# Kernel optimization log

Hardware: AMD Instinct MI355X
Metric: run time of the kernel (lower is better)

Reference implementation:

```python
import jax, jax.numpy as jnp
import numpy as np

W = 5; WW = 25; STEP = 8; DF = 128; NH = 8; DH = 16; EPS = 1e-5


def sinusoid_pe(ww, d):
    pos = np.arange(ww)[:, None].astype(np.float32)
    div = np.exp(np.arange(0, d, 2).astype(np.float32) * (-np.log(10000.0) / d))
    pe = np.zeros((ww, d), np.float32)
    pe[:, 0::2] = np.sin(pos * div)
    pe[:, 1::2] = np.cos(pos * div)
    return jnp.asarray(pe)


def ln(x, s, b):
    m = x.mean(-1, keepdims=True)
    v = ((x - m) ** 2).mean(-1, keepdims=True)
    return (x - m) / jnp.sqrt(v + EPS) * s + b


def attn_layer(x, src, wq, wk, wv, wm, m1w, m1b, m2w, m2b, n1s, n1b, n2s, n2b):
    N, T, D = x.shape
    q = (x @ wq).reshape(N, T, NH, DH)
    k = (src @ wk).reshape(N, T, NH, DH)
    v = (src @ wv).reshape(N, T, NH, DH)
    a = jax.nn.softmax(jnp.einsum('nqhd,nkhd->nhqk', q, k) * (DH ** -0.5), axis=-1)
    msg = jnp.einsum('nhqk,nkhd->nqhd', a, v).reshape(N, T, D) @ wm
    msg = ln(msg, n1s, n1b)
    h = jnp.concatenate([x, msg], axis=-1)
    h = jax.nn.relu(h @ m1w + m1b) @ m2w + m2b
    return x + ln(h, n2s, n2b)


def local_transformer(x0, x1, P):
    names = ['self', 'cross', 'self', 'cross']
    for i, nm in enumerate(names):
        p = tuple(a[i] for a in P)
        if nm == 'self':
            x0 = attn_layer(x0, x0, *p)
            x1 = attn_layer(x1, x1, *p)
        else:
            x0 = attn_layer(x0, x1, *p)
            x1 = attn_layer(x1, x0, *p)
    return x0, x1


def unfold_window(fm):
    # F.unfold(kernel=5, stride=4, pad=2) then 'B (C MM) L -> B L MM C'
    B, C, H, Wd = fm.shape
    pat = jax.lax.conv_general_dilated_patches(fm, (W, W), (4, 4), [(W // 2, W // 2)] * 2)
    Ho, Wo = pat.shape[2], pat.shape[3]
    pat = pat.reshape(B, C, WW, Ho * Wo)  # channel-major ordering matches torch unfold
    return pat.transpose(0, 3, 2, 1)  # [B, L, WW, C]


def forward(mdesc0, mdesc1, fine0, fine1, conv_w, conv_b, proj_w, proj_b,
            merge_w, merge_b, reg1_w, reg1_b, reg2_w, reg2_b, reg_w, reg_b,
            lt_wq, lt_wk, lt_wv, lt_wm, lt_m1w, lt_m1b, lt_m2w, lt_m2b,
            lt_n1s, lt_n1b, lt_n2s, lt_n2b):
    B, L, Dc = mdesc0.shape
    Wc = int(np.sqrt(L))
    # dual-softmax confidence matrix
    sim = jnp.einsum('bld,bmd->blm', mdesc0 / Dc, mdesc1 / Dc) / 0.1
    cm = jax.nn.softmax(sim, axis=1) * jax.nn.softmax(sim, axis=2)
    # mutual nearest-neighbor filter (static-shape: keep all B*L rows + mask)
    mut = (cm == cm.max(axis=2, keepdims=True)) & (cm == cm.max(axis=1, keepdims=True))
    cf = cm * mut
    mask = cf.max(axis=2) > 0  # [B, L]
    j = jnp.argmax(cf, axis=2)  # [B, L]
    # 1x1 conv to fine dim
    f0 = jnp.einsum('bchw,oc->bohw', fine0, conv_w[:, :, 0, 0]) + conv_b[None, :, None, None]
    f1 = jnp.einsum('bchw,oc->bohw', fine1, conv_w[:, :, 0, 0]) + conv_b[None, :, None, None]
    u0 = unfold_window(f0)
    u1 = unfold_window(f1)  # [B, L, WW, DF]
    N = B * L
    b_all = jnp.repeat(jnp.arange(B), L)
    idx1 = b_all * L + j.reshape(-1)
    local0 = u0.reshape(N, WW, DF)
    local1 = u1.reshape(N, WW, DF)[idx1]
    c0 = mdesc0.reshape(N, Dc)
    c1 = mdesc1.reshape(N, Dc)[idx1]
    local = jnp.concatenate([local0, local1], axis=0)  # [2N, WW, DF]
    center = jnp.concatenate([c0, c1], axis=0) @ proj_w + proj_b  # [2N, DF]
    center = jnp.broadcast_to(center[:, None, :], (2 * N, WW, DF))
    ld = jnp.concatenate([local, center], axis=-1) @ merge_w + merge_b
    ld = ld + sinusoid_pe(WW, DF)[None]
    d0, d1 = ld[:N], ld[N:]
    P = (lt_wq, lt_wk, lt_wv, lt_wm, lt_m1w, lt_m1b, lt_m2w, lt_m2b, lt_n1s, lt_n1b, lt_n2s, lt_n2b)
    fd0, fd1 = local_transformer(d0, d1, P)
    c = WW // 2
    cen = jnp.broadcast_to(fd0[:, c:c + 1, :], (N, WW, DF))
    feat = jnp.concatenate([cen, fd1], axis=-1)  # [N, WW, 2*DF]
    feat = feat @ reg1_w + reg1_b  # [N, WW, DF]
    feat = feat.reshape(N, WW * DF)  # [N, 3200]
    feat = feat @ reg2_w + reg2_b  # dropout is identity at eval
    coords = feat @ reg_w + reg_b  # [N, 2]
    xj = (j % Wc) * STEP
    yj = (j // Wc) * STEP
    base = jnp.stack([xj, yj], axis=-1).reshape(N, 2).astype(coords.dtype)
    return (base + coords) * mask.reshape(N, 1).astype(coords.dtype)


def setup_inputs():
    key = jax.random.key(0)
    ks = jax.random.split(key, 24)
    B, L, Dc = 2, 2304, 256
    Hf = 192
    nl = 4

    def rn(k, shape, fan):
        return jax.random.normal(k, shape, jnp.float32) * (fan ** -0.5)

    return {
        'mdesc0': jax.random.normal(ks[0], (B, L, Dc), jnp.float32),
        'mdesc1': jax.random.normal(ks[1], (B, L, Dc), jnp.float32),
        'fine0': jax.random.normal(ks[2], (B, Dc, Hf, Hf), jnp.float32),
        'fine1': jax.random.normal(ks[3], (B, Dc, Hf, Hf), jnp.float32),
        'conv_w': rn(ks[4], (DF, Dc, 1, 1), Dc),
        'conv_b': jnp.zeros((DF,), jnp.float32),
        'proj_w': rn(ks[5], (Dc, DF), Dc),
        'proj_b': jnp.zeros((DF,), jnp.float32),
        'merge_w': rn(ks[6], (2 * DF, DF), 2 * DF),
        'merge_b': jnp.zeros((DF,), jnp.float32),
        'reg1_w': rn(ks[7], (2 * DF, DF), 2 * DF),
        'reg1_b': jnp.zeros((DF,), jnp.float32),
        'reg2_w': rn(ks[8], (WW * DF, DF), WW * DF),
        'reg2_b': jnp.zeros((DF,), jnp.float32),
        'reg_w': rn(ks[9], (DF, 2), DF),
        'reg_b': jnp.zeros((2,), jnp.float32),
        'lt_wq': rn(ks[10], (nl, DF, DF), DF),
        'lt_wk': rn(ks[11], (nl, DF, DF), DF),
        'lt_wv': rn(ks[12], (nl, DF, DF), DF),
        'lt_wm': rn(ks[13], (nl, DF, DF), DF),
        'lt_m1w': rn(ks[14], (nl, 2 * DF, 2 * DF), 2 * DF),
        'lt_m1b': jnp.zeros((nl, 2 * DF), jnp.float32),
        'lt_m2w': rn(ks[15], (nl, 2 * DF, DF), 2 * DF),
        'lt_m2b': jnp.zeros((nl, DF), jnp.float32),
        'lt_n1s': jnp.ones((nl, DF), jnp.float32),
        'lt_n1b': jnp.zeros((nl, DF), jnp.float32),
        'lt_n2s': jnp.ones((nl, DF), jnp.float32),
        'lt_n2b': jnp.zeros((nl, DF), jnp.float32),
    }


def reference(mdesc0, mdesc1, fine0, fine1, conv_w, conv_b, proj_w, proj_b,
              merge_w, merge_b, reg1_w, reg1_b, reg2_w, reg2_b, reg_w, reg_b,
              lt_wq, lt_wk, lt_wv, lt_wm, lt_m1w, lt_m1b, lt_m2w, lt_m2b,
              lt_n1s, lt_n1b, lt_n2s, lt_n2b):
    return forward(mdesc0, mdesc1, fine0, fine1, conv_w, conv_b, proj_w, proj_b,
                   merge_w, merge_b, reg1_w, reg1_b, reg2_w, reg2_b, reg_w, reg_b,
                   lt_wq, lt_wk, lt_wv, lt_wm, lt_m1w, lt_m1b, lt_m2w, lt_m2b,
                   lt_n1s, lt_n1b, lt_n2s, lt_n2b)
```

## Files before the change

### kernel.cpp

```cpp
#include <hip/hip_runtime.h>
#include <stdint.h>
#include <type_traits>

#define DEVFN static __device__ __forceinline__

typedef __attribute__((ext_vector_type(8))) short bf16x8v;
typedef __attribute__((ext_vector_type(4))) float f32x4v;
typedef __attribute__((ext_vector_type(2))) _Float16 h2;

DEVFN float b2f(short s) {
  union { unsigned u; float f; } c; c.u = ((unsigned)(unsigned short)s) << 16; return c.f;
}
DEVFN short f2b(float f) {
  union { float f; unsigned u; } c; c.f = f;
  unsigned r = c.u + 0x7fffu + ((c.u >> 16) & 1u);
  return (short)(r >> 16);
}
DEVFN short f2h(float f) {
  union { _Float16 h; short s; } c; c.h = (_Float16)f; return c.s;
}
DEVFN void gl_lds16(const void* g, void* l) {
  __builtin_amdgcn_global_load_lds((const __attribute__((address_space(1))) void*)g,
                                   (__attribute__((address_space(3))) void*)l, 16, 0, 0);
}
DEVFN double exp_small(double x) {
  return 1.0 + x * (1.0 + x * (0.5 + x * ((1.0 / 6.0) + x * (1.0 / 24.0))));
}


__global__ void prep_all(const float* __restrict__ conv_w, const float* __restrict__ proj_w,
                         const float* __restrict__ merge_w, const float* __restrict__ reg1_w,
                         const float* __restrict__ reg2_w, const float* __restrict__ wq,
                         const float* __restrict__ wk, const float* __restrict__ wv,
                         const float* __restrict__ wm, const float* __restrict__ m1w,
                         const float* __restrict__ m2w,
                         short* __restrict__ convT, short* __restrict__ projT,
                         short* __restrict__ mergeAT, short* __restrict__ mergeBT,
                         short* __restrict__ reg1T, short* __restrict__ reg2T,
                         short* __restrict__ wqkvT, short* __restrict__ wmT,
                         short* __restrict__ m1T, short* __restrict__ m2T,
                         float* __restrict__ pe, short* __restrict__ zp) {
  const int L0 = 32768, L1 = 32768, L2 = 16384, L3 = 16384, L4 = 32768, L5 = 409600;
  const int L6 = 196608, L7 = 65536, L8 = 262144, L9 = 131072, L10 = 3200, L11 = 128;
  const int TOT = L0+L1+L2+L3+L4+L5+L6+L7+L8+L9+L10+L11;
  for (int gi = blockIdx.x * blockDim.x + threadIdx.x; gi < TOT; gi += gridDim.x * blockDim.x) {
    int i = gi;
    if (i < L0) { convT[i] = f2b(conv_w[i]); continue; } i -= L0;
    if (i < L1) { int n = i >> 8, k = i & 255; projT[i] = f2b(proj_w[k * 128 + n]); continue; } i -= L1;
    if (i < L2) { int n = i >> 7, k = i & 127; mergeAT[i] = f2b(merge_w[k * 128 + n]); continue; } i -= L2;
    if (i < L3) { int n = i >> 7, k = i & 127; mergeBT[i] = f2b(merge_w[(128 + k) * 128 + n]); continue; } i -= L3;
    if (i < L4) { int n = i >> 8, k = i & 255; reg1T[i] = f2b(reg1_w[k * 128 + n]); continue; } i -= L4;
    if (i < L5) { int n = i / 3200, k = i - n * 3200; reg2T[i] = f2b(reg2_w[k * 128 + n]); continue; } i -= L5;
    if (i < L6) {
      int l = i / 49152; int r = i - l * 49152; int w = r / 16384; int r2 = r - w * 16384;
      int n = r2 >> 7, k = r2 & 127;
      const float* s = (w == 0) ? wq : (w == 1) ? wk : wv;
      wqkvT[i] = f2b(s[l * 16384 + k * 128 + n]); continue;
    } i -= L6;
    if (i < L7) { int l = i >> 14; int r = i & 16383; int n = r >> 7, k = r & 127;
      wmT[i] = f2b(wm[l * 16384 + k * 128 + n]); continue; } i -= L7;
    if (i < L8) { int l = i >> 16; int r = i & 65535; int n = r >> 8, k = r & 255;
      m1T[i] = f2b(m1w[l * 65536 + k * 256 + n]); continue; } i -= L8;
    if (i < L9) { int l = i >> 15; int r = i & 32767; int n = r >> 8, k = r & 255;
      m2T[i] = f2b(m2w[l * 32768 + k * 128 + n]); continue; } i -= L9;
    if (i < L10) {
      int t = i >> 7, d = i & 127; int i2 = d >> 1;
      float div = expf(((float)(2 * i2)) * (-logf(10000.f) / 128.f));
      float ang = (float)t * div;
      pe[i] = (d & 1) ? cosf(ang) : sinf(ang); continue;
    } i -= L10;
    zp[i] = 0;
  }
}


__global__ __launch_bounds__(256) void sim_gemm(const float* __restrict__ A,
                                                const float* __restrict__ Bm,
                                                float* __restrict__ S) {
  int b = blockIdx.z;
  A += (size_t)b * 2304 * 256; Bm += (size_t)b * 2304 * 256; S += (size_t)b * 2304 * 2304;
  __shared__ float As[96][33], Bs[96][33];
  int tid = threadIdx.x;
  int tx = tid & 15, ty = tid >> 4;
  int rb = blockIdx.x * 96, cb = blockIdx.y * 96;
  float acc[6][6] = {};
  for (int k0 = 0; k0 < 256; k0 += 32) {
    #pragma unroll
    for (int s = 0; s < 3; ++s) {
      int slot = s * 256 + tid;
      int r = slot >> 3, cq = slot & 7;
      float4 va = *(const float4*)&A[(size_t)(rb + r) * 256 + k0 + 4 * cq];
      float4 vb = *(const float4*)&Bm[(size_t)(cb + r) * 256 + k0 + 4 * cq];
      As[r][4 * cq] = va.x; As[r][4 * cq + 1] = va.y; As[r][4 * cq + 2] = va.z; As[r][4 * cq + 3] = va.w;
      Bs[r][4 * cq] = vb.x; Bs[r][4 * cq + 1] = vb.y; Bs[r][4 * cq + 2] = vb.z; Bs[r][4 * cq + 3] = vb.w;
    }
    __syncthreads();
    #pragma unroll 4
    for (int k = 0; k < 32; ++k) {
      float av[6], bv[6];
      #pragma unroll
      for (int i = 0; i < 6; ++i) av[i] = As[ty + 16 * i][k];
      #pragma unroll
      for (int j = 0; j < 6; ++j) bv[j] = Bs[tx + 16 * j][k];
      #pragma unroll
      for (int i = 0; i < 6; ++i)
        #pragma unroll
        for (int j = 0; j < 6; ++j) acc[i][j] += av[i] * bv[j];
    }
    __syncthreads();
  }
  #pragma unroll
  for (int i = 0; i < 6; ++i)
    #pragma unroll
    for (int j = 0; j < 6; ++j) {
      float t = acc[i][j] * (1.0f / 65536.0f);
      S[(size_t)(rb + ty + 16 * i) * 2304 + cb + tx + 16 * j] = t / 0.1f;
    }
}

__global__ __launch_bounds__(256) void row_lse(const float* __restrict__ S, double* __restrict__ lnR) {
  int row = blockIdx.x;
  const float* Sp = S + (size_t)row * 2304;
  double a = 0;
  for (int m = threadIdx.x; m < 2304; m += 256) a += exp_small((double)Sp[m]);
  __shared__ double red[256];
  red[threadIdx.x] = a; __syncthreads();
  for (int s = 128; s > 0; s >>= 1) { if (threadIdx.x < (unsigned)s) red[threadIdx.x] += red[threadIdx.x + s]; __syncthreads(); }
  if (!threadIdx.x) lnR[row] = log(red[0]);
}

__global__ __launch_bounds__(256) void col_part(const float* __restrict__ S,
                                                const double* __restrict__ lnR,
                                                double* __restrict__ psum,
                                                double* __restrict__ pkey,
                                                int* __restrict__ pidx) {
  int bb = blockIdx.z;
  int c0 = blockIdx.x * 64;
  int rc = blockIdx.y;
  int col = c0 + (threadIdx.x & 63);
  int g = threadIdx.x >> 6;
  const float* Sp = S + (size_t)bb * 2304 * 2304;
  const double* lr = lnR + bb * 2304;
  double a = 0, best = -1e300; int bi = 1 << 30;
  int l0 = rc * 192;
  for (int t = g; t < 192; t += 4) {
    int l = l0 + t;
    double sv = (double)Sp[(size_t)l * 2304 + col];
    a += exp_small(sv);
    double k = 2.0 * sv - lr[l];
    if (k > best || (k == best && l < bi)) { best = k; bi = l; }
  }
  __shared__ double s_sum[256]; __shared__ double s_key[256]; __shared__ int s_idx[256];
  s_sum[threadIdx.x] = a; s_key[threadIdx.x] = best; s_idx[threadIdx.x] = bi;
  __syncthreads();
  if (g == 0) {
    double ts = a; double tk = best; int ti = bi;
    #pragma unroll
    for (int gg = 1; gg < 4; ++gg) {
      int o = threadIdx.x + gg * 64;
      ts += s_sum[o];
      if (s_key[o] > tk || (s_key[o] == tk && s_idx[o] < ti)) { tk = s_key[o]; ti = s_idx[o]; }
    }
    size_t off = ((size_t)bb * 12 + rc) * 2304 + col;
    psum[off] = ts; pkey[off] = tk; pidx[off] = ti;
  }
}

__global__ void col_reduce(const double* __restrict__ psum, const double* __restrict__ pkey,
                           const int* __restrict__ pidx, double* __restrict__ lnC,
                           int* __restrict__ CB) {
  int i = blockIdx.x * blockDim.x + threadIdx.x;
  if (i >= 4608) return;
  int bb = i / 2304, col = i - bb * 2304;
  double s = 0; double bk = -1e300; int bi = 1 << 30;
  for (int rc = 0; rc < 12; ++rc) {
    size_t off = ((size_t)bb * 12 + rc) * 2304 + col;
    s += psum[off];
    double k = pkey[off]; int ix = pidx[off];
    if (k > bk || (k == bk && ix < bi)) { bk = k; bi = ix; }
  }
  lnC[i] = log(s);
  CB[i] = bi;
}

__global__ __launch_bounds__(256) void row_argmax(const float* __restrict__ S,
                                                  const double* __restrict__ lnC,
                                                  int* __restrict__ J) {
  int row = blockIdx.x; int bb = row / 2304;
  const float* Sp = S + (size_t)row * 2304;
  const double* lc = lnC + bb * 2304;
  double best = -1e300; int bi = 1 << 30;
  for (int m = threadIdx.x; m < 2304; m += 256) {
    double k = 2.0 * (double)Sp[m] - lc[m];
    if (k > best || (k == best && m < bi)) { best = k; bi = m; }
  }
  __shared__ double bvs[256]; __shared__ int bis[256];
  bvs[threadIdx.x] = best; bis[threadIdx.x] = bi; __syncthreads();
  for (int s = 128; s > 0; s >>= 1) {
    if (threadIdx.x < (unsigned)s) {
      double ov = bvs[threadIdx.x + s]; int oi = bis[threadIdx.x + s];
      if (ov > bvs[threadIdx.x] || (ov == bvs[threadIdx.x] && oi < bis[threadIdx.x])) { bvs[threadIdx.x] = ov; bis[threadIdx.x] = oi; }
    }
    __syncthreads();
  }
  if (!threadIdx.x) J[row] = bis[0];
}


__global__ __launch_bounds__(256) void transpose_fine(const float* __restrict__ src, short* __restrict__ dst) {
  __shared__ float t[64][65];
  int bb = blockIdx.z, p0 = blockIdx.x * 64, c0 = blockIdx.y * 64;
  for (int i = threadIdx.x; i < 4096; i += 256) {
    int cl = i >> 6, pl = i & 63;
    t[cl][pl] = src[((size_t)(bb * 256 + c0 + cl)) * 36864 + p0 + pl];
  }
  __syncthreads();
  for (int i = threadIdx.x; i < 1024; i += 256) {
    int pl = i >> 4, cg = (i & 15) * 4;
    unsigned w0 = (unsigned short)f2b(t[cg][pl]) | ((unsigned)(unsigned short)f2b(t[cg + 1][pl]) << 16);
    unsigned w1 = (unsigned short)f2b(t[cg + 2][pl]) | ((unsigned)(unsigned short)f2b(t[cg + 3][pl]) << 16);
    int2 v; v.x = (int)w0; v.y = (int)w1;
    *(int2*)&dst[((size_t)(bb * 36864 + p0 + pl)) * 256 + c0 + cg] = v;
  }
}

__global__ void cgather(const float* __restrict__ md0, const float* __restrict__ md1,
                        const int* __restrict__ J, short* __restrict__ cbuf) {
  int total = 9216 * 256;
  for (int i = blockIdx.x * blockDim.x + threadIdx.x; i < total; i += gridDim.x * blockDim.x) {
    int w = i >> 8, c = i & 255;
    const float* src;
    if (w < 4608) src = md0 + (size_t)w * 256;
    else {
      int n = w - 4608; int bb = n / 2304;
      src = md1 + (size_t)(bb * 2304 + J[n]) * 256;
    }
    cbuf[i] = f2b(src[c]);
  }
}

__global__ void build_tab(const int* __restrict__ J, const short* __restrict__ f0c,
                          const short* __restrict__ f1c, const short* __restrict__ zp,
                          unsigned long long* __restrict__ tab) {
  int total = 230400;
  for (int i = blockIdx.x * blockDim.x + threadIdx.x; i < total; i += gridDim.x * blockDim.x) {
    int w = i / 25, t = i - w * 25;
    int bb, cell; const short* fc;
    if (w < 4608) { bb = w / 2304; cell = w - bb * 2304; fc = f0c; }
    else { int n = w - 4608; bb = n / 2304; cell = J[n]; fc = f1c; }
    int cy = cell / 48, cx = cell - cy * 48;
    int y = cy * 4 - 2 + t / 5, x = cx * 4 - 2 + t % 5;
    const short* p = (y >= 0 && y < 192 && x >= 0 && x < 192)
                   ? fc + (size_t)((bb * 192 + y) * 192 + x) * 128 : zp;
    tab[i] = (unsigned long long)(uintptr_t)p;
  }
}


constexpr int AM_LIN = 0, AM_DUAL = 1, AM_TAB = 2, AM_CEN = 3, AM_QKV = 4;
constexpr int EP_BIAS = 0, EP_BF32 = 1, EP_RELU = 2, EP_LN = 3, EP_LNRES = 4, EP_MERGE = 5, EP_PART = 6, EP_F16 = 7;

template<int AMODE, int EPI>
__global__ __launch_bounds__(256)
void gemm_bf16(const short* __restrict__ A1, const short* __restrict__ A2,
               const unsigned long long* __restrict__ tab,
               const short* __restrict__ Wt, int M, int Kd, int kstr, int K1,
               const float* __restrict__ bias, int bstride,
               const float* __restrict__ lns, const float* __restrict__ lnb,
               const short* __restrict__ resid,
               const float* __restrict__ ccp, const float* __restrict__ pep,
               short* __restrict__ outb, float* __restrict__ outf, int ldc,
               long wstride, long ostride) {
  __shared__ __align__(16) short As[128 * 64];
  __shared__ __align__(16) short Bs[128 * 64];
  __shared__ float rsum[2][128], rsq[2][128];
  int tid = threadIdx.x, lane = tid & 63, wid = tid >> 6;
  int wr = wid >> 1, wc = wid & 1;
  int nwg = gridDim.x;
  int orig = blockIdx.x;
  int qd = nwg >> 3, rm = nwg & 7;
  int xcd = orig & 7, offx = orig >> 3;
  int bx = (xcd < rm ? xcd * (qd + 1) : rm * (qd + 1) + (xcd - rm) * qd) + offx;
  int rb = bx * 128;
  int by = blockIdx.y;
  int koff = blockIdx.z * Kd;
  const short* Wsel = Wt + (size_t)by * wstride;
  const float* bsel = bias ? bias + (size_t)by * bstride : nullptr;
  short* osel_b = outb ? outb + (size_t)by * ostride : nullptr;
  float* osel_f = outf ? outf + (size_t)by * ostride : nullptr;

  f32x4v acc[4][4];
  #pragma unroll
  for (int i = 0; i < 4; ++i)
    #pragma unroll
    for (int j = 0; j < 4; ++j) acc[i][j] = (f32x4v){0.f, 0.f, 0.f, 0.f};

  for (int k0 = 0; k0 < Kd; k0 += 64) {
    #pragma unroll
    for (int q = 0; q < 4; ++q) {
      int i = (wid * 4 + q) * 64 + lane;
      int r = i >> 3, pch = i & 7;
      int c = pch ^ (r & 7);
      const short* src;
      if (AMODE == AM_LIN) {
        src = A1 + (size_t)(rb + r) * kstr + koff + k0 + c * 8;
      } else if (AMODE == AM_QKV) {
        const short* Ab = (by == 0) ? A1 : A2;
        src = Ab + (size_t)(rb + r) * kstr + k0 + c * 8;
      } else if (AMODE == AM_DUAL) {
        if (k0 < K1) src = A1 + (size_t)(rb + r) * K1 + k0 + c * 8;
        else         src = A2 + (size_t)(rb + r) * (Kd - K1) + (k0 - K1) + c * 8;
      } else if (AMODE == AM_CEN) {
        int rg = rb + r;
        if (k0 < K1) src = A1 + (size_t)((rg / 25) * 25 + 12) * K1 + k0 + c * 8;
        else         src = A2 + (size_t)rg * (Kd - K1) + (k0 - K1) + c * 8;
      } else {
        src = (const short*)(uintptr_t)tab[rb + r] + k0 + c * 8;
      }
      gl_lds16(src, &As[(size_t)i * 8]);
    }
    #pragma unroll
    for (int q = 0; q < 4; ++q) {
      int i = (wid * 4 + q) * 64 + lane;
      int r = i >> 3, pch = i & 7;
      int c = pch ^ (r & 7);
      gl_lds16(Wsel + (size_t)r * kstr + koff + k0 + c * 8, &Bs[(size_t)i * 8]);
    }
    __syncthreads();
    #pragma unroll
    for (int kk = 0; kk < 2; ++kk) {
      bf16x8v af[4], bfr[4];
      #pragma unroll
      for (int mi = 0; mi < 4; ++mi) {
        int r = wr * 64 + mi * 16 + (lane & 15);
        int c = kk * 4 + (lane >> 4);
        int pch = c ^ (r & 7);
        af[mi] = *(const bf16x8v*)&As[r * 64 + pch * 8];
      }
      #pragma unroll
      for (int ni = 0; ni < 4; ++ni) {
        int r = wc * 64 + ni * 16 + (lane & 15);
        int c = kk * 4 + (lane >> 4);
        int pch = c ^ (r & 7);
        bfr[ni] = *(const bf16x8v*)&Bs[r * 64 + pch * 8];
      }
      #pragma unroll
      for (int mi = 0; mi < 4; ++mi)
        #pragma unroll
        for (int ni = 0; ni < 4; ++ni)
          acc[mi][ni] = __builtin_amdgcn_mfma_f32_16x16x32_bf16(af[mi], bfr[ni], acc[mi][ni], 0, 0, 0);
    }
    __syncthreads();
  }

  int colloc[4];
  #pragma unroll
  for (int ni = 0; ni < 4; ++ni) colloc[ni] = wc * 64 + ni * 16 + (lane & 15);
  float bv[4];
  #pragma unroll
  for (int ni = 0; ni < 4; ++ni)
    bv[ni] = (EPI == EP_MERGE || EPI == EP_PART) ? 0.f : (bsel ? bsel[colloc[ni]] : 0.f);

  #pragma unroll
  for (int mi = 0; mi < 4; ++mi)
    #pragma unroll
    for (int ni = 0; ni < 4; ++ni)
      #pragma unroll
      for (int q = 0; q < 4; ++q) {
        float v = acc[mi][ni][q] + bv[ni];
        if (EPI == EP_RELU) v = fmaxf(v, 0.f);
        acc[mi][ni][q] = v;
      }

  if (EPI == EP_LN || EPI == EP_LNRES) {
    #pragma unroll
    for (int mi = 0; mi < 4; ++mi)
      #pragma unroll
      for (int q = 0; q < 4; ++q) {
        float s = 0.f, ss = 0.f;
        #pragma unroll
        for (int ni = 0; ni < 4; ++ni) { float v = acc[mi][ni][q]; s += v; ss += v * v; }
        s += __shfl_xor(s, 1, 64); ss += __shfl_xor(ss, 1, 64);
        s += __shfl_xor(s, 2, 64); ss += __shfl_xor(ss, 2, 64);
        s += __shfl_xor(s, 4, 64); ss += __shfl_xor(ss, 4, 64);
        s += __shfl_xor(s, 8, 64); ss += __shfl_xor(ss, 8, 64);
        int rl = wr * 64 + mi * 16 + (lane >> 4) * 4 + q;
        if ((lane & 15) == 0) { rsum[wc][rl] = s; rsq[wc][rl] = ss; }
      }
    __syncthreads();
  }

  #pragma unroll
  for (int mi = 0; mi < 4; ++mi)
    #pragma unroll
    for (int q = 0; q < 4; ++q) {
      int rl = wr * 64 + mi * 16 + (lane >> 4) * 4 + q;
      long rg = rb + rl;
      float mean = 0.f, rstd = 0.f;
      if (EPI == EP_LN || EPI == EP_LNRES) {
        float s = rsum[0][rl] + rsum[1][rl];
        float ss = rsq[0][rl] + rsq[1][rl];
        mean = s * (1.f / 128.f);
        float var = ss * (1.f / 128.f) - mean * mean;
        rstd = 1.f / sqrtf(var + 1e-5f);
      }
      int wv_ = 0, tv_ = 0;
      if (EPI == EP_MERGE) { wv_ = (int)(rg / 25); tv_ = (int)(rg - (long)wv_ * 25); }
      #pragma unroll
      for (int ni = 0; ni < 4; ++ni) {
        int cg = colloc[ni];
        float v = acc[mi][ni][q];
        if (EPI == EP_MERGE) v += ccp[(size_t)wv_ * 128 + cg] + pep[tv_ * 128 + cg];
        if (EPI == EP_LN || EPI == EP_LNRES) {
          v = (v - mean) * rstd * lns[cg] + lnb[cg];
          if (EPI == EP_LNRES) v += b2f(resid[(size_t)rg * 128 + cg]);
        }
        if (EPI == EP_BF32) osel_f[(size_t)rg * ldc + cg] = v;
        else if (EPI == EP_PART) osel_f[((size_t)blockIdx.z * M + rg) * ldc + cg] = v;
        else if (EPI == EP_F16) osel_b[(size_t)rg * ldc + cg] = f2h(v);
        else osel_b[(size_t)rg * ldc + cg] = f2b(v);
      }
    }
}

__global__ void reduce_part(const float* __restrict__ part, const float* __restrict__ bias,
                            short* __restrict__ out) {
  int i = blockIdx.x * blockDim.x + threadIdx.x;
  if (i >= 4608 * 128) return;
  int c = i & 127;
  float s = bias[c];
  #pragma unroll
  for (int z = 0; z < 5; ++z) s += part[(size_t)z * 4608 * 128 + i];
  out[i] = f2b(s);
}


__global__ __launch_bounds__(256) void attn_win(const short* __restrict__ Q,
                                                const short* __restrict__ K,
                                                const short* __restrict__ V,
                                                short* __restrict__ Mo) {
  int w = blockIdx.x;
  const short* Qg = Q + (size_t)w * 3200;
  const short* Kg = K + (size_t)w * 3200;
  const short* Vg = V + (size_t)w * 3200;
  __shared__ short Qs[25 * 136 + 8], Ks[25 * 136 + 8], Vs[25 * 136 + 8];
  int tid = threadIdx.x;
  for (int s = tid; s < 400; s += 256) {
    int r = s >> 4, ch = s & 15;
    *(int4*)&Qs[r * 136 + ch * 8] = ((const int4*)Qg)[s];
    *(int4*)&Ks[r * 136 + ch * 8] = ((const int4*)Kg)[s];
    *(int4*)&Vs[r * 136 + ch * 8] = ((const int4*)Vg)[s];
  }
  __syncthreads();

  int wid = tid >> 6, lane = tid & 63;
  int half = lane >> 5, li = lane & 31;
  int h = wid * 2 + half;
  if (li < 25) {
    int i = li;
    h2 qr[8];
    #pragma unroll
    for (int t = 0; t < 8; ++t) qr[t] = *(const h2*)&Qs[i * 136 + h * 16 + t * 2];
    float p[25];
    float mx = -1e30f;
    #pragma unroll
    for (int jx = 0; jx < 25; ++jx) {
      const short* kr = &Ks[jx * 136 + h * 16];
      float s = 0.f;
      #pragma unroll
      for (int t = 0; t < 8; ++t)
        s = __builtin_amdgcn_fdot2(qr[t], *(const h2*)&kr[t * 2], s, false);
      s *= 0.25f;
      p[jx] = s;
      mx = fmaxf(mx, s);
    }
    float sum = 0.f;
    #pragma unroll
    for (int jx = 0; jx < 25; ++jx) { float e = expf(p[jx] - mx); p[jx] = e; sum += e; }
    float inv = 1.f / sum;
    h2 o2[8];
    #pragma unroll
    for (int t = 0; t < 8; ++t) { o2[t][0] = (_Float16)0.f; o2[t][1] = (_Float16)0.f; }
    #pragma unroll
    for (int jx = 0; jx < 25; ++jx) {
      _Float16 ph = (_Float16)(p[jx] * inv);
      h2 pv; pv[0] = ph; pv[1] = ph;
      const short* vr = &Vs[jx * 136 + h * 16];
      #pragma unroll
      for (int t = 0; t < 8; ++t) o2[t] += pv * (*(const h2*)&vr[t * 2]);
    }
    int* outp = (int*)(Mo + (size_t)w * 3200 + i * 128 + h * 16);
    #pragma unroll
    for (int t = 0; t < 8; ++t) {
      unsigned lo = (unsigned short)f2b((float)o2[t][0]);
      unsigned hi = (unsigned short)f2b((float)o2[t][1]);
      outp[t] = (int)(lo | (hi << 16));
    }
  }
}


__global__ void final_reg(const short* __restrict__ fv, const float* __restrict__ regw,
                          const float* __restrict__ regb, const int* __restrict__ J,
                          const int* __restrict__ CB, float* __restrict__ out) {
  int n = blockIdx.x * blockDim.x + threadIdx.x;
  if (n >= 4608) return;
  const short* f = fv + (size_t)n * 128;
  float c0 = regb[0], c1 = regb[1];
  for (int d = 0; d < 128; ++d) { float v = b2f(f[d]); c0 += v * regw[d * 2]; c1 += v * regw[d * 2 + 1]; }
  int jv = J[n]; int bb = n / 2304;
  int msk = (CB[bb * 2304 + jv] == (n - bb * 2304)) ? 1 : 0;
  float bx = (float)((jv % 48) * 8), by = (float)((jv / 48) * 8);
  out[n * 2] = msk ? (bx + c0) : 0.f;
  out[n * 2 + 1] = msk ? (by + c1) : 0.f;
}


extern "C" void kernel_launch(void* const* d_in, const int* in_sizes, int n_in,
                              void* d_out, int out_size, void* d_ws, size_t ws_size,
                              hipStream_t stream) {
  const float* md0 = (const float*)d_in[0];
  const float* md1 = (const float*)d_in[1];
  const float* fine0 = (const float*)d_in[2];
  const float* fine1 = (const float*)d_in[3];
  const float* conv_w = (const float*)d_in[4];
  const float* conv_b = (const float*)d_in[5];
  const float* proj_w = (const float*)d_in[6];
  const float* proj_b = (const float*)d_in[7];
  const float* merge_w = (const float*)d_in[8];
  const float* merge_b = (const float*)d_in[9];
  const float* reg1_w = (const float*)d_in[10];
  const float* reg1_b = (const float*)d_in[11];
  const float* reg2_w = (const float*)d_in[12];
  const float* reg2_b = (const float*)d_in[13];
  const float* reg_w = (const float*)d_in[14];
  const float* reg_b = (const float*)d_in[15];
  const float* wq_f = (const float*)d_in[16];
  const float* wk_f = (const float*)d_in[17];
  const float* wv_f = (const float*)d_in[18];
  const float* wm_f = (const float*)d_in[19];
  const float* m1w = (const float*)d_in[20];
  const float* m1b = (const float*)d_in[21];
  const float* m2w = (const float*)d_in[22];
  const float* m2b = (const float*)d_in[23];
  const float* n1s = (const float*)d_in[24];
  const float* n1b = (const float*)d_in[25];
  const float* n2s = (const float*)d_in[26];
  const float* n2b = (const float*)d_in[27];

  char* ws = (char*)d_ws;
  const size_t SZX = (size_t)230400 * 128 * 2;
  const size_t TAILSZ = 20 * 1024 * 1024;
  int CHM = 57600;
  if (SZX + 4ull * 230400 * 256 + TAILSZ <= ws_size)      CHM = 230400;
  else if (SZX + 4ull * 115200 * 256 + TAILSZ <= ws_size) CHM = 115200;
  const size_t CHR = (size_t)CHM * 256;

  short* X  = (short*)(ws);
  char*  Rb = ws + SZX;
  short* R0 = (short*)(Rb);
  short* R1 = (short*)(Rb + CHR);
  short* R2 = (short*)(Rb + 2 * CHR);
  short* R3 = (short*)(Rb + 3 * CHR);
  float* S    = (float*)Rb;
  short* F0C  = (short*)Rb;
  short* F1C  = (short*)(Rb + (size_t)73728 * 128 * 2);
  short* FT   = X;
  short* FB   = (short*)Rb;
  float* PART = (float*)(Rb + 2 * CHR);

  char* p = ws + SZX + 4 * CHR;
  double* lnR = (double*)p; p += 4608 * 8;
  double* lnC = (double*)p; p += 4608 * 8;
  int* J = (int*)p; p += 4608 * 4;
  int* CBst = (int*)p; p += 4608 * 4;
  double* PSUM = (double*)p; p += (size_t)2 * 12 * 2304 * 8;
  double* PKEY = (double*)p; p += (size_t)2 * 12 * 2304 * 8;
  int* PIDX = (int*)p; p += (size_t)2 * 12 * 2304 * 4;
  short* CBUF = (short*)p; p += (size_t)9216 * 256 * 2;
  short* CEN = (short*)p; p += (size_t)9216 * 128 * 2;
  float* CC = (float*)p; p += (size_t)9216 * 128 * 4;
  unsigned long long* TAB = (unsigned long long*)p; p += (size_t)230400 * 8;
  float* PE = (float*)p; p += 3200 * 4;
  short* ZP = (short*)p; p += 256;
  short* convT = (short*)p; p += 128 * 256 * 2;
  short* projT = (short*)p; p += 128 * 256 * 2;
  short* mergeAT = (short*)p; p += 128 * 128 * 2;
  short* mergeBT = (short*)p; p += 128 * 128 * 2;
  short* reg1T = (short*)p; p += 128 * 256 * 2;
  short* reg2T = (short*)p; p += (size_t)128 * 3200 * 2;
  short* wqkvT = (short*)p; p += (size_t)4 * 3 * 128 * 128 * 2;
  short* wmT = (short*)p; p += 4 * 128 * 128 * 2;
  short* m1T = (short*)p; p += 4 * 256 * 256 * 2;
  short* m2T = (short*)p; p += (size_t)4 * 128 * 256 * 2;
  short* FV = (short*)p; p += (size_t)4608 * 128 * 2;

  const int TQ = 115200;

  prep_all<<<512, 256, 0, stream>>>(conv_w, proj_w, merge_w, reg1_w, reg2_w,
                                    wq_f, wk_f, wv_f, wm_f, m1w, m2w,
                                    convT, projT, mergeAT, mergeBT, reg1T, reg2T,
                                    wqkvT, wmT, m1T, m2T, PE, ZP);

  sim_gemm<<<dim3(24, 24, 2), 256, 0, stream>>>(md0, md1, S);
  row_lse<<<4608, 256, 0, stream>>>(S, lnR);
  col_part<<<dim3(36, 12, 2), 256, 0, stream>>>(S, lnR, PSUM, PKEY, PIDX);
  col_reduce<<<18, 256, 0, stream>>>(PSUM, PKEY, PIDX, lnC, CBst);
  row_argmax<<<4608, 256, 0, stream>>>(S, lnC, J);

  auto gemm = [&](auto amode, auto epi, const short* A1, const short* A2,
                  const unsigned long long* tab, const short* Wt, int M, int Kd, int kstr, int K1,
                  const float* bias, int bstride, const float* lns, const float* lnb,
                  const short* resid, const float* cc, const float* pe,
                  short* outb, float* outf, int ldc, int NB, int NZ, long wstride, long ostride) {
    constexpr int AM = decltype(amode)::value, EP = decltype(epi)::value;
    gemm_bf16<AM, EP><<<dim3(M / 128, NB, NZ), 256, 0, stream>>>(
        A1, A2, tab, Wt, M, Kd, kstr, K1, bias, bstride, lns, lnb, resid, cc, pe,
        outb, outf, ldc, wstride, ostride);
  };
  using I0 = std::integral_constant<int, 0>; using I1 = std::integral_constant<int, 1>;
  using I2 = std::integral_constant<int, 2>; using I3 = std::integral_constant<int, 3>;
  using I4 = std::integral_constant<int, 4>;
  using E0 = std::integral_constant<int, 0>; using E1 = std::integral_constant<int, 1>;
  using E2 = std::integral_constant<int, 2>; using E3 = std::integral_constant<int, 3>;
  using E4 = std::integral_constant<int, 4>; using E5 = std::integral_constant<int, 5>;
  using E6 = std::integral_constant<int, 6>; using E7 = std::integral_constant<int, 7>;

  transpose_fine<<<dim3(576, 4, 2), 256, 0, stream>>>(fine0, FT);
  gemm(I0{}, E0{}, FT, nullptr, nullptr, convT, 73728, 256, 256, 0, conv_b, 0, nullptr, nullptr, nullptr, nullptr, nullptr, F0C, nullptr, 128, 1, 1, 0, 0);
  transpose_fine<<<dim3(576, 4, 2), 256, 0, stream>>>(fine1, FT);
  gemm(I0{}, E0{}, FT, nullptr, nullptr, convT, 73728, 256, 256, 0, conv_b, 0, nullptr, nullptr, nullptr, nullptr, nullptr, F1C, nullptr, 128, 1, 1, 0, 0);

  cgather<<<4608, 256, 0, stream>>>(md0, md1, J, CBUF);
  gemm(I0{}, E0{}, CBUF, nullptr, nullptr, projT, 9216, 256, 256, 0, proj_b, 0, nullptr, nullptr, nullptr, nullptr, nullptr, CEN, nullptr, 128, 1, 1, 0, 0);
  gemm(I0{}, E1{}, CEN, nullptr, nullptr, mergeBT, 9216, 128, 128, 0, merge_b, 0, nullptr, nullptr, nullptr, nullptr, nullptr, nullptr, CC, 128, 1, 1, 0, 0);
  build_tab<<<900, 256, 0, stream>>>(J, F0C, F1C, ZP, TAB);
  gemm(I2{}, E5{}, nullptr, nullptr, TAB, mergeAT, 230400, 128, 128, 0, nullptr, 0, nullptr, nullptr, nullptr, CC, PE, X, nullptr, 128, 1, 1, 0, 0);

  auto pass = [&](int i, const short* xq, const short* xkv, short* xout, int Mtotal) {
    const short* wqkv = wqkvT + (size_t)i * 3 * 16384;
    const short* wm = wmT + i * 16384;
    const short* m1 = m1T + i * 65536;
    const short* m2 = m2T + i * 32768;
    for (int off = 0; off < Mtotal; off += CHM) {
      int Mc = (Mtotal - off < CHM) ? (Mtotal - off) : CHM;
      const short* xqc = xq + (size_t)off * 128;
      const short* xkvc = xkv + (size_t)off * 128;
      gemm(I4{}, E7{}, xqc, xkvc, nullptr, wqkv, Mc, 128, 128, 0, nullptr, 0, nullptr, nullptr, nullptr, nullptr, nullptr, R0, nullptr, 128, 3, 1, 16384, (long)CHM * 128);
      attn_win<<<Mc / 25, 256, 0, stream>>>(R0, R1, R2, R0);
      gemm(I0{}, E3{}, R0, nullptr, nullptr, wm, Mc, 128, 128, 0, nullptr, 0, n1s + i * 128, n1b + i * 128, nullptr, nullptr, nullptr, R3, nullptr, 128, 1, 1, 0, 0);
      gemm(I1{}, E2{}, xqc, R3, nullptr, m1, Mc, 256, 256, 128, m1b + i * 256, 128, nullptr, nullptr, nullptr, nullptr, nullptr, R0, nullptr, 256, 2, 1, 128 * 256, 128);
      gemm(I0{}, E4{}, R0, nullptr, nullptr, m2, Mc, 256, 256, 0, m2b + i * 128, 0, n2s + i * 128, n2b + i * 128, xqc, nullptr, nullptr, xout + (size_t)off * 128, nullptr, 128, 1, 1, 0, 0);
    }
  };
  short* X1 = X + (size_t)TQ * 128;
  for (int i = 0; i < 4; ++i) {
    if ((i & 1) == 0) {
      pass(i, X, X, X, 230400);
    } else {
      pass(i, X, X1, X, TQ);
      pass(i, X1, X, X1, TQ);
    }
  }

  gemm(I3{}, E0{}, X, X1, nullptr, reg1T, TQ, 256, 256, 128, reg1_b, 0, nullptr, nullptr, nullptr, nullptr, nullptr, FB, nullptr, 128, 1, 1, 0, 0);
  gemm(I0{}, E6{}, FB, nullptr, nullptr, reg2T, 4608, 640, 3200, 0, nullptr, 0, nullptr, nullptr, nullptr, nullptr, nullptr, nullptr, PART, 128, 1, 5, 0, 0);
  reduce_part<<<2304, 256, 0, stream>>>(PART, reg2_b, FV);
  final_reg<<<18, 256, 0, stream>>>(FV, reg_w, reg_b, J, CBst, (float*)d_out);
}
```

Before: 1.772 ms.

## Fuse MLP up/down projections with LayerNorm residual into one kernel

Replaces the two GEMM launches for the attention-layer MLP (concat[x,msg]·m1 + relu, then ·m2 + bias, LayerNorm and residual) with one kernel. Each 64-row block keeps the 256-wide hidden activation in LDS in two 128-column halves and accumulates the second GEMM directly, so the hidden tensor never goes through global memory. In exchange the GEMM tiling is hand-written with less pipelining, and Mc must be a multiple of 64 since the grid is Mc/64 with no tail handling. In-place output (xout == xqc) is safe only if each block reads its own x rows before writing them.

Result: faster. 1.669 ms (-5.8%).

```diff
diff --git a/kernel.cpp b/kernel.cpp
--- a/kernel.cpp
+++ b/kernel.cpp
@@ -435,6 +435,184 @@
 }
 
 
+__global__ __launch_bounds__(256)
+void mlp_fused(const short* __restrict__ x, const short* __restrict__ msg,
+               const short* __restrict__ m1wT, const short* __restrict__ m2wT,
+               const float* __restrict__ b1, const float* __restrict__ b2,
+               const float* __restrict__ lns, const float* __restrict__ lnb,
+               short* __restrict__ out) {
+  __shared__ __align__(16) short As[64 * 64];
+  __shared__ __align__(16) short Bs[128 * 64];
+  __shared__ __align__(16) short Hs[64 * 128];
+  __shared__ float rsum[2][64], rsq[2][64];
+  int tid = threadIdx.x, lane = tid & 63, wid = tid >> 6;
+  int wr = wid >> 1, wc = wid & 1;
+  int nwg = gridDim.x;
+  int orig = blockIdx.x;
+  int qd = nwg >> 3, rm = nwg & 7;
+  int xcd = orig & 7, offx = orig >> 3;
+  int bx = (xcd < rm ? xcd * (qd + 1) : rm * (qd + 1) + (xcd - rm) * qd) + offx;
+  int rb = bx * 64;
+
+  f32x4v acc2[2][4];
+  #pragma unroll
+  for (int i = 0; i < 2; ++i)
+    #pragma unroll
+    for (int j = 0; j < 4; ++j) acc2[i][j] = (f32x4v){0.f, 0.f, 0.f, 0.f};
+
+  #pragma unroll
+  for (int nh = 0; nh < 2; ++nh) {
+    f32x4v acc1[2][4];
+    #pragma unroll
+    for (int i = 0; i < 2; ++i)
+      #pragma unroll
+      for (int j = 0; j < 4; ++j) acc1[i][j] = (f32x4v){0.f, 0.f, 0.f, 0.f};
+
+    for (int k0 = 0; k0 < 256; k0 += 64) {
+      #pragma unroll
+      for (int q = 0; q < 2; ++q) {
+        int i = (wid * 2 + q) * 64 + lane;
+        int r = i >> 3, pch = i & 7;
+        int c = pch ^ (r & 7);
+        const short* src = (k0 < 128)
+            ? x + (size_t)(rb + r) * 128 + k0 + c * 8
+            : msg + (size_t)(rb + r) * 128 + (k0 - 128) + c * 8;
+        gl_lds16(src, &As[(size_t)i * 8]);
+      }
+      #pragma unroll
+      for (int q = 0; q < 4; ++q) {
+        int i = (wid * 4 + q) * 64 + lane;
+        int r = i >> 3, pch = i & 7;
+        int c = pch ^ (r & 7);
+        gl_lds16(m1wT + (size_t)(nh * 128 + r) * 256 + k0 + c * 8, &Bs[(size_t)i * 8]);
+      }
+      __syncthreads();
+      #pragma unroll
+      for (int kk = 0; kk < 2; ++kk) {
+        bf16x8v af[2], bfr[4];
+        #pragma unroll
+        for (int mi = 0; mi < 2; ++mi) {
+          int r = wr * 32 + mi * 16 + (lane & 15);
+          int c = kk * 4 + (lane >> 4);
+          int pch = c ^ (r & 7);
+          af[mi] = *(const bf16x8v*)&As[r * 64 + pch * 8];
+        }
+        #pragma unroll
+        for (int ni = 0; ni < 4; ++ni) {
+          int r = wc * 64 + ni * 16 + (lane & 15);
+          int c = kk * 4 + (lane >> 4);
+          int pch = c ^ (r & 7);
+          bfr[ni] = *(const bf16x8v*)&Bs[r * 64 + pch * 8];
+        }
+        #pragma unroll
+        for (int mi = 0; mi < 2; ++mi)
+          #pragma unroll
+          for (int ni = 0; ni < 4; ++ni)
+            acc1[mi][ni] = __builtin_amdgcn_mfma_f32_16x16x32_bf16(af[mi], bfr[ni], acc1[mi][ni], 0, 0, 0);
+      }
+      __syncthreads();
+    }
+    #pragma unroll
+    for (int mi = 0; mi < 2; ++mi)
+      #pragma unroll
+      for (int q = 0; q < 4; ++q) {
+        int rl = wr * 32 + mi * 16 + (lane >> 4) * 4 + q;
+        #pragma unroll
+        for (int ni = 0; ni < 4; ++ni) {
+          int cg = wc * 64 + ni * 16 + (lane & 15);
+          float v = fmaxf(acc1[mi][ni][q] + b1[nh * 128 + cg], 0.f);
+          int c = cg >> 3, pch = c ^ (rl & 7);
+          Hs[rl * 128 + pch * 8 + (cg & 7)] = f2b(v);
+        }
+      }
+    __syncthreads();
+
+    #pragma unroll
+    for (int k2 = 0; k2 < 2; ++k2) {
+      #pragma unroll
+      for (int q = 0; q < 4; ++q) {
+        int i = (wid * 4 + q) * 64 + lane;
+        int r = i >> 3, pch = i & 7;
+        int c = pch ^ (r & 7);
+        gl_lds16(m2wT + (size_t)r * 256 + nh * 128 + k2 * 64 + c * 8, &Bs[(size_t)i * 8]);
+      }
+      __syncthreads();
+      #pragma unroll
+      for (int kk = 0; kk < 2; ++kk) {
+        bf16x8v af[2], bfr[4];
+        #pragma unroll
+        for (int mi = 0; mi < 2; ++mi) {
+          int r = wr * 32 + mi * 16 + (lane & 15);
+          int cH = k2 * 8 + kk * 4 + (lane >> 4);
+          int pch = cH ^ (r & 7);
+          af[mi] = *(const bf16x8v*)&Hs[r * 128 + pch * 8];
+        }
+        #pragma unroll
+        for (int ni = 0; ni < 4; ++ni) {
+          int r = wc * 64 + ni * 16 + (lane & 15);
+          int c = kk * 4 + (lane >> 4);
+          int pch = c ^ (r & 7);
+          bfr[ni] = *(const bf16x8v*)&Bs[r * 64 + pch * 8];
+        }
+        #pragma unroll
+        for (int mi = 0; mi < 2; ++mi)
+          #pragma unroll
+          for (int ni = 0; ni < 4; ++ni)
+            acc2[mi][ni] = __builtin_amdgcn_mfma_f32_16x16x32_bf16(af[mi], bfr[ni], acc2[mi][ni], 0, 0, 0);
+      }
+      __syncthreads();
+    }
+  }
+
+  int colloc[4];
+  #pragma unroll
+  for (int ni = 0; ni < 4; ++ni) colloc[ni] = wc * 64 + ni * 16 + (lane & 15);
+  #pragma unroll
+  for (int mi = 0; mi < 2; ++mi)
+    #pragma unroll
+    for (int ni = 0; ni < 4; ++ni)
+      #pragma unroll
+      for (int q = 0; q < 4; ++q)
+        acc2[mi][ni][q] += b2[colloc[ni]];
+
+  #pragma unroll
+  for (int mi = 0; mi < 2; ++mi)
+    #pragma unroll
+    for (int q = 0; q < 4; ++q) {
+      float s = 0.f, ss = 0.f;
+      #pragma unroll
+      for (int ni = 0; ni < 4; ++ni) { float v = acc2[mi][ni][q]; s += v; ss += v * v; }
+      s += __shfl_xor(s, 1, 64); ss += __shfl_xor(ss, 1, 64);
+      s += __shfl_xor(s, 2, 64); ss += __shfl_xor(ss, 2, 64);
+      s += __shfl_xor(s, 4, 64); ss += __shfl_xor(ss, 4, 64);
+      s += __shfl_xor(s, 8, 64); ss += __shfl_xor(ss, 8, 64);
+      int rl = wr * 32 + mi * 16 + (lane >> 4) * 4 + q;
+      if ((lane & 15) == 0) { rsum[wc][rl] = s; rsq[wc][rl] = ss; }
+    }
+  __syncthreads();
+
+  #pragma unroll
+  for (int mi = 0; mi < 2; ++mi)
+    #pragma unroll
+    for (int q = 0; q < 4; ++q) {
+      int rl = wr * 32 + mi * 16 + (lane >> 4) * 4 + q;
+      long rg = rb + rl;
+      float s = rsum[0][rl] + rsum[1][rl];
+      float ss = rsq[0][rl] + rsq[1][rl];
+      float mean = s * (1.f / 128.f);
+      float var = ss * (1.f / 128.f) - mean * mean;
+      float rstd = 1.f / sqrtf(var + 1e-5f);
+      #pragma unroll
+      for (int ni = 0; ni < 4; ++ni) {
+        int cg = colloc[ni];
+        float v = (acc2[mi][ni][q] - mean) * rstd * lns[cg] + lnb[cg];
+        v += b2f(x[(size_t)rg * 128 + cg]);
+        out[(size_t)rg * 128 + cg] = f2b(v);
+      }
+    }
+}
+
+
 __global__ __launch_bounds__(256) void attn_win(const short* __restrict__ Q,
                                                 const short* __restrict__ K,
                                                 const short* __restrict__ V,
@@ -649,8 +827,9 @@
       gemm(I4{}, E7{}, xqc, xkvc, nullptr, wqkv, Mc, 128, 128, 0, nullptr, 0, nullptr, nullptr, nullptr, nullptr, nullptr, R0, nullptr, 128, 3, 1, 16384, (long)CHM * 128);
       attn_win<<<Mc / 25, 256, 0, stream>>>(R0, R1, R2, R0);
       gemm(I0{}, E3{}, R0, nullptr, nullptr, wm, Mc, 128, 128, 0, nullptr, 0, n1s + i * 128, n1b + i * 128, nullptr, nullptr, nullptr, R3, nullptr, 128, 1, 1, 0, 0);
-      gemm(I1{}, E2{}, xqc, R3, nullptr, m1, Mc, 256, 256, 128, m1b + i * 256, 128, nullptr, nullptr, nullptr, nullptr, nullptr, R0, nullptr, 256, 2, 1, 128 * 256, 128);
-      gemm(I0{}, E4{}, R0, nullptr, nullptr, m2, Mc, 256, 256, 0, m2b + i * 128, 0, n2s + i * 128, n2b + i * 128, xqc, nullptr, nullptr, xout + (size_t)off * 128, nullptr, 128, 1, 1, 0, 0);
+      mlp_fused<<<Mc / 64, 256, 0, stream>>>(xqc, R3, m1, m2, m1b + i * 256, m2b + i * 128,
+                                             n2s + i * 128, n2b + i * 128,
+                                             xout + (size_t)off * 128);
     }
   };
   short* X1 = X + (size_t)TQ * 128;
```
